# Kernel optimization log

Hardware: AMD Instinct MI355X
Metric: run time of the kernel (lower is better)

## Reference

```python
import jax, jax.numpy as jnp
import numpy as np

B, T, D = 4, 2048, 1024
H, S = 16, 64  # n_heads, stalk_dim; D == H*S
P_ADIC_BASE = 2
MAX_VAL = 16


def quantize_6bit(x):
    # symmetric int6 quantization with straight-through estimator
    scale = jnp.max(jnp.abs(x)) / 31.0 + 1e-8
    q = jnp.clip(jnp.round(x / scale), -31, 31) * scale
    return x + jax.lax.stop_gradient(q - x)


def build_p_adic_bias(seq_len, p=2, max_val=16):
    idx = jnp.arange(seq_len)
    d = jnp.abs(idx[:, None] - idx[None, :])
    nonzero = d > 0
    vp = jnp.zeros_like(d)
    work = d
    for _ in range(max_val):  # fixed iterations; v_2(|i-j|) <= log2(T) < 16
        divisible = nonzero & (work % p == 0)
        vp = vp + divisible.astype(vp.dtype)
        work = jnp.where(divisible, work // p, work)
    vals = jnp.minimum(vp, max_val).astype(jnp.float32)
    vals = jnp.where(nonzero, vals, jnp.float32(max_val))
    return vals / max_val


def setup_inputs() -> dict:
    key = jax.random.key(0)
    ks = jax.random.split(key, 8)
    std = 0.02
    return {
        "x": jax.random.normal(ks[0], (B, T, D), dtype=jnp.float32),
        "wq": jax.random.normal(ks[1], (D, D), dtype=jnp.float32) * std,
        "wk": jax.random.normal(ks[2], (D, D), dtype=jnp.float32) * std,
        "wv": jax.random.normal(ks[3], (D, D), dtype=jnp.float32) * std,
        "wo": jax.random.normal(ks[4], (D, D), dtype=jnp.float32) * std,
        "wu": jax.random.normal(ks[5], (S, S), dtype=jnp.float32) * std,
        "wsv": jax.random.normal(ks[6], (S, S), dtype=jnp.float32) * std,
        "p_scale": jnp.ones((1,), dtype=jnp.float32) * 0.1,
    }


def reference(x, wq, wk, wv, wo, wu, wsv, p_scale):
    h, s = H, S
    scale = 1.0 / jnp.sqrt(jnp.float32(s))
    # quantized linear projections (F.linear: x @ W.T)
    Q = (x @ quantize_6bit(wq).T).reshape(B, T, h, s).transpose(0, 2, 1, 3)
    K = (x @ quantize_6bit(wk).T).reshape(B, T, h, s).transpose(0, 2, 1, 3)
    V = (x @ quantize_6bit(wv).T).reshape(B, T, h, s).transpose(0, 2, 1, 3)
    # stalk (low-rank sheaf) maps on the head dim
    Qs = Q @ quantize_6bit(wu).T
    Ks = K @ quantize_6bit(wsv).T
    scores = jnp.einsum("bhqs,bhks->bhqk", Qs, Ks) * scale
    p_bias = build_p_adic_bias(T, p=P_ADIC_BASE, max_val=MAX_VAL)
    scores = scores + p_scale[0] * p_bias[None, None, :, :]
    causal = jnp.triu(jnp.ones((T, T), dtype=bool), k=1)
    scores = jnp.where(causal[None, None], -jnp.inf, scores)
    attn = jax.nn.softmax(scores, axis=-1)
    out = jnp.einsum("bhqk,bhks->bhqs", attn, V)
    out = out.transpose(0, 2, 1, 3).reshape(B, T, D)
    return out @ quantize_6bit(wo).T
```

## Files before the change

### kernel.cpp

```cpp
#include <hip/hip_runtime.h>
#include <hip/hip_bf16.h>
#include <stdint.h>


typedef __bf16 bf16_t;
typedef __attribute__((ext_vector_type(4))) __bf16 bf16x4;
typedef __attribute__((ext_vector_type(8))) __bf16 bf16x8;
typedef __attribute__((ext_vector_type(4))) float f32x4;

#define BB 4
#define TT 2048
#define DD 1024
#define HH 16
#define SS 64

__device__ __forceinline__ float quant6(float v, float s) {
    float q = rintf(v / s);
    q = fminf(fmaxf(q, -31.0f), 31.0f);
    return q * s;
}

__device__ __forceinline__ float fexp2(float x) {
#if __has_builtin(__builtin_amdgcn_exp2f)
    return __builtin_amdgcn_exp2f(x);
#else
    return exp2f(x);
#endif
}

typedef __attribute__((address_space(3))) uint32_t lds_u32;
typedef const __attribute__((address_space(1))) uint32_t glb_u32;

__global__ __launch_bounds__(256) void absmax6(const float* __restrict__ wq,
                                               const float* __restrict__ wk,
                                               const float* __restrict__ wv,
                                               const float* __restrict__ wo,
                                               const float* __restrict__ wu,
                                               const float* __restrict__ wsv,
                                               float* __restrict__ amax) {
    const int t = blockIdx.y;
    const float* src = (t == 0) ? wq : (t == 1) ? wk : (t == 2) ? wv
                     : (t == 3) ? wo : (t == 4) ? wu : wsv;
    const int n4 = (t < 4) ? (1048576 / 4) : (4096 / 4);
    float m = 0.0f;
    for (int i = blockIdx.x * blockDim.x + threadIdx.x; i < n4; i += gridDim.x * blockDim.x) {
        float4 v = ((const float4*)src)[i];
        m = fmaxf(m, fmaxf(fmaxf(fabsf(v.x), fabsf(v.y)), fmaxf(fabsf(v.z), fabsf(v.w))));
    }
    #pragma unroll
    for (int mask = 32; mask > 0; mask >>= 1)
        m = fmaxf(m, __shfl_xor(m, mask));
    __shared__ float red[4];
    int w = threadIdx.x >> 6;
    if ((threadIdx.x & 63) == 0) red[w] = m;
    __syncthreads();
    if (threadIdx.x == 0) {
        m = fmaxf(fmaxf(red[0], red[1]), fmaxf(red[2], red[3]));
        atomicMax((int*)(amax + t), __float_as_int(m));
    }
}

__global__ __launch_bounds__(256) void xcvt_kernel(const float* __restrict__ x,
                                                   bf16_t* __restrict__ xb) {
    int i = (blockIdx.x * 256 + threadIdx.x) * 8;
    float4 f0 = *(const float4*)(x + i);
    float4 f1 = *(const float4*)(x + i + 4);
    bf16x8 v;
    v[0] = (bf16_t)f0.x; v[1] = (bf16_t)f0.y; v[2] = (bf16_t)f0.z; v[3] = (bf16_t)f0.w;
    v[4] = (bf16_t)f1.x; v[5] = (bf16_t)f1.y; v[6] = (bf16_t)f1.z; v[7] = (bf16_t)f1.w;
    *(bf16x8*)(xb + i) = v;
}

__global__ __launch_bounds__(256) void prep_w(const float* __restrict__ wq,
                                              const float* __restrict__ wk,
                                              const float* __restrict__ wv,
                                              const float* __restrict__ wo,
                                              const float* __restrict__ wu,
                                              const float* __restrict__ wsv,
                                              const float* __restrict__ amax,
                                              bf16_t* __restrict__ W_all,
                                              bf16_t* __restrict__ Wo) {
    const int which = blockIdx.y;
    if (blockIdx.x < 512) {
        const float* src = which ? wo : wv;
        bf16_t* dst = which ? Wo : (W_all + (size_t)2048 * 1024);
        float s = amax[which ? 3 : 2] / 31.0f + 1e-8f;
        int i = (blockIdx.x * 256 + threadIdx.x) * 8;
        float4 f0 = *(const float4*)(src + i);
        float4 f1 = *(const float4*)(src + i + 4);
        bf16x8 v;
        v[0] = (bf16_t)quant6(f0.x, s); v[1] = (bf16_t)quant6(f0.y, s);
        v[2] = (bf16_t)quant6(f0.z, s); v[3] = (bf16_t)quant6(f0.w, s);
        v[4] = (bf16_t)quant6(f1.x, s); v[5] = (bf16_t)quant6(f1.y, s);
        v[6] = (bf16_t)quant6(f1.z, s); v[7] = (bf16_t)quant6(f1.w, s);
        *(bf16x8*)(dst + i) = v;
        return;
    }
    const int fx = blockIdx.x - 512;
    const float* wbig = which ? wk : wq;
    const float* wsml = which ? wsv : wu;
    const float sb = amax[which ? 1 : 0] / 31.0f + 1e-8f;
    const float ss = amax[which ? 5 : 4] / 31.0f + 1e-8f;
    const float oscale = which ? 1.0f : 0.125f * 1.44269504089f;
    bf16_t* outp = W_all + (size_t)which * 1024 * 1024;
    const int h = fx >> 4, n0 = (fx & 15) * 64;
    const int w = threadIdx.x >> 6, l = threadIdx.x & 63;
    const int l15 = l & 15, quad = l >> 4, q8 = quad * 8;
    const int m0 = w * 16;

    bf16x8 af[2];
    #pragma unroll
    for (int kc = 0; kc < 2; ++kc) {
        const float* src = wsml + (m0 + l15) * 64 + kc * 32 + q8;
        float4 f0 = *(const float4*)(src);
        float4 f1 = *(const float4*)(src + 4);
        bf16x8 a;
        a[0] = (bf16_t)quant6(f0.x, ss); a[1] = (bf16_t)quant6(f0.y, ss);
        a[2] = (bf16_t)quant6(f0.z, ss); a[3] = (bf16_t)quant6(f0.w, ss);
        a[4] = (bf16_t)quant6(f1.x, ss); a[5] = (bf16_t)quant6(f1.y, ss);
        a[6] = (bf16_t)quant6(f1.z, ss); a[7] = (bf16_t)quant6(f1.w, ss);
        af[kc] = a;
    }
    f32x4 acc[4];
    #pragma unroll
    for (int nb = 0; nb < 4; ++nb) acc[nb] = (f32x4){0.f, 0.f, 0.f, 0.f};
    #pragma unroll
    for (int kc = 0; kc < 2; ++kc) {
        #pragma unroll
        for (int nb = 0; nb < 4; ++nb) {
            bf16x8 bfr;
            #pragma unroll
            for (int j = 0; j < 8; ++j)
                bfr[j] = (bf16_t)quant6(wbig[(size_t)(h * 64 + kc * 32 + q8 + j) * 1024 + n0 + nb * 16 + l15], sb);
            acc[nb] = __builtin_amdgcn_mfma_f32_16x16x32_bf16(af[kc], bfr, acc[nb], 0, 0, 0);
        }
    }
    #pragma unroll
    for (int nb = 0; nb < 4; ++nb)
        #pragma unroll
        for (int r = 0; r < 4; ++r)
            outp[(size_t)(h * 64 + m0 + quad * 4 + r) * 1024 + n0 + nb * 16 + l15] =
                (bf16_t)(acc[nb][r] * oscale);
}

template <bool OUT_F32>
__global__ __launch_bounds__(256) void gemm128(const bf16_t* __restrict__ A,
                                               const bf16_t* __restrict__ Bt,
                                               void* __restrict__ Cv,
                                               int lda, int ldb, int ldc, int K) {
    __shared__ __align__(16) bf16_t As[128 * 64];
    __shared__ __align__(16) bf16_t Bs[128 * 64];
    const int tid = threadIdx.x;
    const int w = tid >> 6, l = tid & 63;
    const int l15 = l & 15, quad = l >> 4;
    const int m0 = blockIdx.y * 128, n0 = blockIdx.x * 128;
    const int wm = (w & 1) * 64, wn = (w >> 1) * 64;

    f32x4 acc[4][4];
    #pragma unroll
    for (int a = 0; a < 4; ++a)
        #pragma unroll
        for (int b = 0; b < 4; ++b) acc[a][b] = (f32x4){0.f, 0.f, 0.f, 0.f};

    for (int kc = 0; kc < K; kc += 64) {
        __syncthreads();
        #pragma unroll
        for (int rep = 0; rep < 4; ++rep) {
            int ci = rep * 256 + w * 64 + l;
            int row = ci >> 3, slot = ci & 7;
            int gch = slot ^ ((row ^ (row >> 3)) & 7);
            __builtin_amdgcn_global_load_lds(
                (glb_u32*)(A + (size_t)(m0 + row) * lda + kc + gch * 8),
                (lds_u32*)(As + (rep * 256 + w * 64) * 8), 16, 0, 0);
            __builtin_amdgcn_global_load_lds(
                (glb_u32*)(Bt + (size_t)(n0 + row) * ldb + kc + gch * 8),
                (lds_u32*)(Bs + (rep * 256 + w * 64) * 8), 16, 0, 0);
        }
        __syncthreads();
        #pragma unroll
        for (int kb = 0; kb < 2; ++kb) {
            bf16x8 af[4], bfr[4];
            #pragma unroll
            for (int mb = 0; mb < 4; ++mb) {
                int row = wm + mb * 16 + l15;
                int slot = ((kb << 2) + quad) ^ ((row ^ (row >> 3)) & 7);
                af[mb] = *(const bf16x8*)(As + (row << 6) + slot * 8);
            }
            #pragma unroll
            for (int nb = 0; nb < 4; ++nb) {
                int row = wn + nb * 16 + l15;
                int slot = ((kb << 2) + quad) ^ ((row ^ (row >> 3)) & 7);
                bfr[nb] = *(const bf16x8*)(Bs + (row << 6) + slot * 8);
            }
            #pragma unroll
            for (int mb = 0; mb < 4; ++mb)
                #pragma unroll
                for (int nb = 0; nb < 4; ++nb)
                    acc[mb][nb] = __builtin_amdgcn_mfma_f32_16x16x32_bf16(af[mb], bfr[nb], acc[mb][nb], 0, 0, 0);
        }
    }
    #pragma unroll
    for (int mb = 0; mb < 4; ++mb) {
        #pragma unroll
        for (int nb = 0; nb < 4; ++nb) {
            int col = n0 + wn + nb * 16 + l15;
            #pragma unroll
            for (int r = 0; r < 4; ++r) {
                int row = m0 + wm + mb * 16 + quad * 4 + r;
                if constexpr (OUT_F32)
                    ((float*)Cv)[(size_t)row * ldc + col] = acc[mb][nb][r];
                else
                    ((bf16_t*)Cv)[(size_t)row * ldc + col] = (bf16_t)acc[mb][nb][r];
            }
        }
    }
}

__global__ __launch_bounds__(256) void vtrans_kernel(const bf16_t* __restrict__ QKV,
                                                     bf16_t* __restrict__ Vt) {
    __shared__ __align__(16) bf16_t tile[64 * 72];
    const int tid = threadIdx.x;
    const int bh = blockIdx.x >> 5, tt = blockIdx.x & 31;
    const int b = bh >> 4, h = bh & 15;
    #pragma unroll
    for (int rep = 0; rep < 2; ++rep) {
        int ci = rep * 256 + tid;
        int row = ci >> 3, ch = ci & 7;
        bf16x8 v = *(const bf16x8*)(QKV + ((size_t)(b * TT + tt * 64 + row)) * 3072 + 2048 + h * 64 + ch * 8);
        #pragma unroll
        for (int j = 0; j < 8; ++j) tile[(ch * 8 + j) * 72 + row] = v[j];
    }
    __syncthreads();
    #pragma unroll
    for (int rep = 0; rep < 2; ++rep) {
        int ci = rep * 256 + tid;
        int s = ci >> 3, ch = ci & 7;
        bf16x8 v = *(const bf16x8*)(tile + s * 72 + ch * 8);
        *(bf16x8*)(Vt + ((size_t)(bh * 64 + s)) * TT + tt * 64 + ch * 8) = v;
    }
}

__device__ __forceinline__ void attn_step(bf16_t* __restrict__ Pw,
                                          const bf16x8 kb[4][2], const bf16x8 vb[4][2],
                                          const bf16x8 qa[2],
                                          f32x4* oacc, float& lrun,
                                          int qlane, int kbase, bool diag, float pb2,
                                          int l15, int quad) {
    f32x4 sacc[4];
    #pragma unroll
    for (int c = 0; c < 4; ++c) sacc[c] = (f32x4){0.f, 0.f, 0.f, 0.f};
    #pragma unroll
    for (int kc = 0; kc < 2; ++kc)
        #pragma unroll
        for (int c = 0; c < 4; ++c)
            sacc[c] = __builtin_amdgcn_mfma_f32_16x16x32_bf16(kb[c][kc], qa[kc], sacc[c], 0, 0, 0);

    const int kp0 = kbase + quad * 4;
    #pragma unroll
    for (int c = 0; c < 4; ++c) {
        bf16x4 pk;
        #pragma unroll
        for (int r = 0; r < 4; ++r) {
            const int k = kp0 + c * 16 + r;
            const int d = qlane - k;
            float ctzf = (float)__builtin_ctz((unsigned)d | 0x10000u);
            float s2 = sacc[c][r] + pb2 * ctzf;
            if (diag && k > qlane) s2 = -INFINITY;
            float p = fexp2(s2);
            lrun += p;
            pk[r] = (bf16_t)p;
        }
        int pp = (c * 2 + (quad >> 1)) ^ (l15 & 7);
        *(bf16x4*)(Pw + l15 * 64 + pp * 8 + (quad & 1) * 4) = pk;
    }
    __builtin_amdgcn_wave_barrier();
    #pragma unroll
    for (int kc = 0; kc < 2; ++kc) {
        bf16x8 pa = *(const bf16x8*)(Pw + l15 * 64 + (((kc * 4 + quad) ^ (l15 & 7)) * 8));
        #pragma unroll
        for (int sb = 0; sb < 4; ++sb)
            oacc[sb] = __builtin_amdgcn_mfma_f32_16x16x32_bf16(pa, vb[sb][kc], oacc[sb], 0, 0, 0);
    }
    __builtin_amdgcn_wave_barrier();
}

__global__ __launch_bounds__(256, 2) void attn_kernel(const bf16_t* __restrict__ QKV,
                                                      const bf16_t* __restrict__ Vt,
                                                      const float* __restrict__ p_scale_ptr,
                                                      bf16_t* __restrict__ O) {
    __shared__ __align__(16) bf16_t Ks[2][64 * 64];
    __shared__ __align__(16) bf16_t Vs[2][64 * 64];
    __shared__ __align__(16) bf16_t Ps[4 * 16 * 64];

    const int tid = threadIdx.x;
    const int w = tid >> 6, l = tid & 63;
    const int l15 = l & 15, quad = l >> 4, q8 = quad * 8;
    const int pair = (blockIdx.x >> 3) & 15;
    const int bh = (blockIdx.x & 7) + ((blockIdx.x >> 7) << 3);
    const int b = bh >> 4, h = bh & 15;
    const int qtA = pair, qtB = 31 - pair;
    const int q0A = qtA * 64 + w * 16, q0B = qtB * 64 + w * 16;
    const int qlA = q0A + l15, qlB = q0B + l15;

    const float pb2 = p_scale_ptr[0] * 1.44269504089f * 0.0625f;
    const size_t xbase = (size_t)b * TT * 3072;

    const int srow = tid >> 3, sslot = tid & 7;
    const int sgch = sslot ^ ((srow ^ (srow >> 3)) & 7);
    const int srow2 = (tid + 256) >> 3, sslot2 = tid & 7;
    const int sgch2 = sslot2 ^ ((srow2 ^ (srow2 >> 3)) & 7);
    const bf16_t* Kg = QKV + xbase + 1024 + h * 64;
    const bf16_t* Vg = Vt + (size_t)bh * 131072;

    bf16x8 qaA[2], qaB[2];
    #pragma unroll
    for (int kc = 0; kc < 2; ++kc) {
        qaA[kc] = *(const bf16x8*)(QKV + xbase + (size_t)(q0A + l15) * 3072 + h * 64 + kc * 32 + q8);
        qaB[kc] = *(const bf16x8*)(QKV + xbase + (size_t)(q0B + l15) * 3072 + h * 64 + kc * 32 + q8);
    }

    f32x4 oA[4], oB[4];
    float lA = 0.f, lB = 0.f;
    #pragma unroll
    for (int i = 0; i < 4; ++i) {
        oA[i] = (f32x4){0.f, 0.f, 0.f, 0.f};
        oB[i] = (f32x4){0.f, 0.f, 0.f, 0.f};
    }
    bf16_t* Pw = Ps + w * 1024;

    {
        const int kbase = 0;
        __builtin_amdgcn_global_load_lds((glb_u32*)(Kg + (size_t)(kbase + srow) * 3072 + sgch * 8),
                                         (lds_u32*)(Ks[0] + (tid >> 3) * 64 + 0), 16, 0, 0);
    }

    {
        #pragma unroll
        for (int rep = 0; rep < 2; ++rep) {
            int ci = rep * 256 + tid;
            int row = ci >> 3, slot = ci & 7;
            int gch = slot ^ ((row ^ (row >> 3)) & 7);
            __builtin_amdgcn_global_load_lds(
                (glb_u32*)(Kg + (size_t)row * 3072 + gch * 8),
                (lds_u32*)(Ks[0] + (rep * 256 + w * 64) * 8), 16, 0, 0);
            __builtin_amdgcn_global_load_lds(
                (glb_u32*)(Vg + (size_t)row * 2048 + gch * 8),
                (lds_u32*)(Vs[0] + (rep * 256 + w * 64) * 8), 16, 0, 0);
        }
    }

    for (int kt = 0; kt <= qtB; ++kt) {
        const int cur = kt & 1;
        __syncthreads();
        if (kt < qtB) {
            const int kbase1 = (kt + 1) * 64;
            const int nxt = cur ^ 1;
            #pragma unroll
            for (int rep = 0; rep < 2; ++rep) {
                int ci = rep * 256 + tid;
                int row = ci >> 3, slot = ci & 7;
                int gch = slot ^ ((row ^ (row >> 3)) & 7);
                __builtin_amdgcn_global_load_lds(
                    (glb_u32*)(Kg + (size_t)(kbase1 + row) * 3072 + gch * 8),
                    (lds_u32*)(Ks[nxt] + (rep * 256 + w * 64) * 8), 16, 0, 0);
                __builtin_amdgcn_global_load_lds(
                    (glb_u32*)(Vg + (size_t)row * 2048 + kbase1 + gch * 8),
                    (lds_u32*)(Vs[nxt] + (rep * 256 + w * 64) * 8), 16, 0, 0);
            }
        }
        const int kbase = kt * 64;
        bf16x8 kb[4][2], vb[4][2];
        #pragma unroll
        for (int kc = 0; kc < 2; ++kc) {
            #pragma unroll
            for (int c = 0; c < 4; ++c) {
                int row = c * 16 + l15;
                int slot = (kc * 4 + quad) ^ ((row ^ (row >> 3)) & 7);
                kb[c][kc] = *(const bf16x8*)(Ks[cur] + row * 64 + slot * 8);
                vb[c][kc] = *(const bf16x8*)(Vs[cur] + row * 64 + slot * 8);
            }
        }
        attn_step(Pw, kb, vb, qaB, oB, lB, qlB, kbase, kt == qtB, pb2, l15, quad);
        if (kt <= qtA)
            attn_step(Pw, kb, vb, qaA, oA, lA, qlA, kbase, kt == qtA, pb2, l15, quad);
    }

    #pragma unroll
    for (int t = 0; t < 2; ++t) {
        float s = t ? lB : lA;
        f32x4* oo = t ? oB : oA;
        int q0 = t ? q0B : q0A;
        s += __shfl_xor(s, 16);
        s += __shfl_xor(s, 32);
        float inv = 1.0f / s;
        #pragma unroll
        for (int r = 0; r < 4; ++r) {
            float invr = __shfl(inv, quad * 4 + r);
            #pragma unroll
            for (int sb = 0; sb < 4; ++sb) {
                int q = q0 + quad * 4 + r;
                int col = h * 64 + sb * 16 + l15;
                O[(size_t)(b * TT + q) * DD + col] = (bf16_t)(oo[sb][r] * invr);
            }
        }
    }
}

extern "C" void kernel_launch(void* const* d_in, const int* in_sizes, int n_in,
                              void* d_out, int out_size, void* d_ws, size_t ws_size,
                              hipStream_t stream) {
    const float* x   = (const float*)d_in[0];
    const float* wq  = (const float*)d_in[1];
    const float* wk  = (const float*)d_in[2];
    const float* wv  = (const float*)d_in[3];
    const float* wo  = (const float*)d_in[4];
    const float* wu  = (const float*)d_in[5];
    const float* wsv = (const float*)d_in[6];
    const float* psc = (const float*)d_in[7];
    float* out = (float*)d_out;

    char* ws = (char*)d_ws;
    float*  amax  = (float*)(ws);
    bf16_t* W_all = (bf16_t*)(ws + 256);
    bf16_t* Wo    = (bf16_t*)(ws + 6291712);
    bf16_t* xb    = (bf16_t*)(ws + 8388864);
    bf16_t* Obuf  = xb;
    bf16_t* QKV   = (bf16_t*)(ws + 25166080);
    bf16_t* Vt    = (bf16_t*)(ws + 75497728);

    hipLaunchKernelGGL(absmax6, dim3(64, 6), dim3(256), 0, stream, wq, wk, wv, wo, wu, wsv, amax);
    hipLaunchKernelGGL(prep_w, dim3(768, 2), dim3(256), 0, stream,
                       wq, wk, wv, wo, wu, wsv, amax, W_all, Wo);
    hipLaunchKernelGGL(xcvt_kernel, dim3(4096), dim3(256), 0, stream, x, xb);

    hipLaunchKernelGGL((gemm128<false>), dim3(24, 64), dim3(256), 0, stream,
                       xb, W_all, (void*)QKV, 1024, 1024, 3072, 1024);

    hipLaunchKernelGGL(vtrans_kernel, dim3(2048), dim3(256), 0, stream, QKV, Vt);

    hipLaunchKernelGGL(attn_kernel, dim3(1024), dim3(256), 0, stream, QKV, Vt, psc, Obuf);

    hipLaunchKernelGGL((gemm128<true>), dim3(8, 64), dim3(256), 0, stream,
                       Obuf, Wo, (void*)out, 1024, 1024, 1024, 1024);
}
```

Baseline: 290.8 us.

## Use two waves per attention block, each handling 32 query rows

The attention kernel drops from four waves to two per block. Each wave now owns two 16-row query sub-tiles per query tile, so every K/V fragment read from LDS is reused across twice as many query rows. K/V tile staging is spread over 128 threads with four load repetitions, and the per-wave P scratch shrinks accordingly. The cost is double the accumulator and Q register state per wave, which may raise register pressure and reduce occupancy. Fewer waves are also available to hide latency.

Result: slower. 316.6 us (+8.9%).

```diff
diff --git a/kernel.cpp b/kernel.cpp
--- a/kernel.cpp
+++ b/kernel.cpp
@@ -284,13 +284,13 @@
     __builtin_amdgcn_wave_barrier();
 }
 
-__global__ __launch_bounds__(256, 2) void attn_kernel(const bf16_t* __restrict__ QKV,
+__global__ __launch_bounds__(128, 2) void attn_kernel(const bf16_t* __restrict__ QKV,
                                                       const bf16_t* __restrict__ Vt,
                                                       const float* __restrict__ p_scale_ptr,
                                                       bf16_t* __restrict__ O) {
     __shared__ __align__(16) bf16_t Ks[2][64 * 64];
     __shared__ __align__(16) bf16_t Vs[2][64 * 64];
-    __shared__ __align__(16) bf16_t Ps[4 * 16 * 64];
+    __shared__ __align__(16) bf16_t Ps[2 * 16 * 64];
 
     const int tid = threadIdx.x;
     const int w = tid >> 6, l = tid & 63;
@@ -299,54 +299,46 @@
     const int bh = (blockIdx.x & 7) + ((blockIdx.x >> 7) << 3);
     const int b = bh >> 4, h = bh & 15;
     const int qtA = pair, qtB = 31 - pair;
-    const int q0A = qtA * 64 + w * 16, q0B = qtB * 64 + w * 16;
-    const int qlA = q0A + l15, qlB = q0B + l15;
 
     const float pb2 = p_scale_ptr[0] * 1.44269504089f * 0.0625f;
     const size_t xbase = (size_t)b * TT * 3072;
-
-    const int srow = tid >> 3, sslot = tid & 7;
-    const int sgch = sslot ^ ((srow ^ (srow >> 3)) & 7);
-    const int srow2 = (tid + 256) >> 3, sslot2 = tid & 7;
-    const int sgch2 = sslot2 ^ ((srow2 ^ (srow2 >> 3)) & 7);
     const bf16_t* Kg = QKV + xbase + 1024 + h * 64;
     const bf16_t* Vg = Vt + (size_t)bh * 131072;
 
-    bf16x8 qaA[2], qaB[2];
-    #pragma unroll
-    for (int kc = 0; kc < 2; ++kc) {
-        qaA[kc] = *(const bf16x8*)(QKV + xbase + (size_t)(q0A + l15) * 3072 + h * 64 + kc * 32 + q8);
-        qaB[kc] = *(const bf16x8*)(QKV + xbase + (size_t)(q0B + l15) * 3072 + h * 64 + kc * 32 + q8);
-    }
-
-    f32x4 oA[4], oB[4];
-    float lA = 0.f, lB = 0.f;
-    #pragma unroll
-    for (int i = 0; i < 4; ++i) {
-        oA[i] = (f32x4){0.f, 0.f, 0.f, 0.f};
-        oB[i] = (f32x4){0.f, 0.f, 0.f, 0.f};
-    }
+    bf16x8 qaA[2][2], qaB[2][2];
+    #pragma unroll
+    for (int rs = 0; rs < 2; ++rs) {
+        #pragma unroll
+        for (int kc = 0; kc < 2; ++kc) {
+            qaA[rs][kc] = *(const bf16x8*)(QKV + xbase +
+                (size_t)(qtA * 64 + w * 32 + rs * 16 + l15) * 3072 + h * 64 + kc * 32 + q8);
+            qaB[rs][kc] = *(const bf16x8*)(QKV + xbase +
+                (size_t)(qtB * 64 + w * 32 + rs * 16 + l15) * 3072 + h * 64 + kc * 32 + q8);
+        }
+    }
+
+    f32x4 oA[2][4], oB[2][4];
+    float lA[2] = {0.f, 0.f}, lB[2] = {0.f, 0.f};
+    #pragma unroll
+    for (int rs = 0; rs < 2; ++rs)
+        #pragma unroll
+        for (int i = 0; i < 4; ++i) {
+            oA[rs][i] = (f32x4){0.f, 0.f, 0.f, 0.f};
+            oB[rs][i] = (f32x4){0.f, 0.f, 0.f, 0.f};
+        }
     bf16_t* Pw = Ps + w * 1024;
 
-    {
-        const int kbase = 0;
-        __builtin_amdgcn_global_load_lds((glb_u32*)(Kg + (size_t)(kbase + srow) * 3072 + sgch * 8),
-                                         (lds_u32*)(Ks[0] + (tid >> 3) * 64 + 0), 16, 0, 0);
-    }
-
-    {
-        #pragma unroll
-        for (int rep = 0; rep < 2; ++rep) {
-            int ci = rep * 256 + tid;
-            int row = ci >> 3, slot = ci & 7;
-            int gch = slot ^ ((row ^ (row >> 3)) & 7);
-            __builtin_amdgcn_global_load_lds(
-                (glb_u32*)(Kg + (size_t)row * 3072 + gch * 8),
-                (lds_u32*)(Ks[0] + (rep * 256 + w * 64) * 8), 16, 0, 0);
-            __builtin_amdgcn_global_load_lds(
-                (glb_u32*)(Vg + (size_t)row * 2048 + gch * 8),
-                (lds_u32*)(Vs[0] + (rep * 256 + w * 64) * 8), 16, 0, 0);
-        }
+    #pragma unroll
+    for (int rep = 0; rep < 4; ++rep) {
+        int ci = rep * 128 + tid;
+        int row = ci >> 3, slot = ci & 7;
+        int gch = slot ^ ((row ^ (row >> 3)) & 7);
+        __builtin_amdgcn_global_load_lds(
+            (glb_u32*)(Kg + (size_t)row * 3072 + gch * 8),
+            (lds_u32*)(Ks[0] + (rep * 128 + w * 64) * 8), 16, 0, 0);
+        __builtin_amdgcn_global_load_lds(
+            (glb_u32*)(Vg + (size_t)row * 2048 + gch * 8),
+            (lds_u32*)(Vs[0] + (rep * 128 + w * 64) * 8), 16, 0, 0);
     }
 
     for (int kt = 0; kt <= qtB; ++kt) {
@@ -356,16 +348,16 @@
             const int kbase1 = (kt + 1) * 64;
             const int nxt = cur ^ 1;
             #pragma unroll
-            for (int rep = 0; rep < 2; ++rep) {
-                int ci = rep * 256 + tid;
+            for (int rep = 0; rep < 4; ++rep) {
+                int ci = rep * 128 + tid;
                 int row = ci >> 3, slot = ci & 7;
                 int gch = slot ^ ((row ^ (row >> 3)) & 7);
                 __builtin_amdgcn_global_load_lds(
                     (glb_u32*)(Kg + (size_t)(kbase1 + row) * 3072 + gch * 8),
-                    (lds_u32*)(Ks[nxt] + (rep * 256 + w * 64) * 8), 16, 0, 0);
+                    (lds_u32*)(Ks[nxt] + (rep * 128 + w * 64) * 8), 16, 0, 0);
                 __builtin_amdgcn_global_load_lds(
                     (glb_u32*)(Vg + (size_t)row * 2048 + kbase1 + gch * 8),
-                    (lds_u32*)(Vs[nxt] + (rep * 256 + w * 64) * 8), 16, 0, 0);
+                    (lds_u32*)(Vs[nxt] + (rep * 128 + w * 64) * 8), 16, 0, 0);
             }
         }
         const int kbase = kt * 64;
@@ -380,27 +372,37 @@
                 vb[c][kc] = *(const bf16x8*)(Vs[cur] + row * 64 + slot * 8);
             }
         }
-        attn_step(Pw, kb, vb, qaB, oB, lB, qlB, kbase, kt == qtB, pb2, l15, quad);
-        if (kt <= qtA)
-            attn_step(Pw, kb, vb, qaA, oA, lA, qlA, kbase, kt == qtA, pb2, l15, quad);
+        #pragma unroll
+        for (int rs = 0; rs < 2; ++rs)
+            attn_step(Pw, kb, vb, qaB[rs], oB[rs], lB[rs],
+                      qtB * 64 + w * 32 + rs * 16 + l15, kbase, kt == qtB, pb2, l15, quad);
+        if (kt <= qtA) {
+            #pragma unroll
+            for (int rs = 0; rs < 2; ++rs)
+                attn_step(Pw, kb, vb, qaA[rs], oA[rs], lA[rs],
+                          qtA * 64 + w * 32 + rs * 16 + l15, kbase, kt == qtA, pb2, l15, quad);
+        }
     }
 
     #pragma unroll
     for (int t = 0; t < 2; ++t) {
-        float s = t ? lB : lA;
-        f32x4* oo = t ? oB : oA;
-        int q0 = t ? q0B : q0A;
-        s += __shfl_xor(s, 16);
-        s += __shfl_xor(s, 32);
-        float inv = 1.0f / s;
-        #pragma unroll
-        for (int r = 0; r < 4; ++r) {
-            float invr = __shfl(inv, quad * 4 + r);
-            #pragma unroll
-            for (int sb = 0; sb < 4; ++sb) {
-                int q = q0 + quad * 4 + r;
-                int col = h * 64 + sb * 16 + l15;
-                O[(size_t)(b * TT + q) * DD + col] = (bf16_t)(oo[sb][r] * invr);
+        #pragma unroll
+        for (int rs = 0; rs < 2; ++rs) {
+            float s = t ? lB[rs] : lA[rs];
+            f32x4* oo = t ? oB[rs] : oA[rs];
+            int q0 = (t ? qtB : qtA) * 64 + w * 32 + rs * 16;
+            s += __shfl_xor(s, 16);
+            s += __shfl_xor(s, 32);
+            float inv = 1.0f / s;
+            #pragma unroll
+            for (int r = 0; r < 4; ++r) {
+                float invr = __shfl(inv, quad * 4 + r);
+                #pragma unroll
+                for (int sb = 0; sb < 4; ++sb) {
+                    int q = q0 + quad * 4 + r;
+                    int col = h * 64 + sb * 16 + l15;
+                    O[(size_t)(b * TT + q) * DD + col] = (bf16_t)(oo[sb][r] * invr);
+                }
             }
         }
     }
@@ -438,7 +440,7 @@
 
     hipLaunchKernelGGL(vtrans_kernel, dim3(2048), dim3(256), 0, stream, QKV, Vt);
 
-    hipLaunchKernelGGL(attn_kernel, dim3(1024), dim3(256), 0, stream, QKV, Vt, psc, Obuf);
+    hipLaunchKernelGGL(attn_kernel, dim3(1024), dim3(128), 0, stream, QKV, Vt, psc, Obuf);
 
     hipLaunchKernelGGL((gemm128<true>), dim3(8, 64), dim3(256), 0, stream,
                        Obuf, Wo, (void*)out, 1024, 1024, 1024, 1024);
```
